# Kernel optimization log

Measured on AMD Instinct MI355X. Metric: run time of the kernel, lower is better.

Reference implementation:

```python
import jax, jax.numpy as jnp
import numpy as np

N_NODES = 100000
N_EDGES = 1600000
DIM_IN, DIM_HID, DIM_OUT = 64, 128, 40


def setup_inputs() -> dict:
    key = jax.random.key(0)
    ks = jax.random.split(key, 6)
    x = jax.random.normal(ks[0], (N_NODES, DIM_IN), dtype=jnp.float32)
    edge_index = jax.random.randint(ks[1], (2, N_EDGES), 0, N_NODES, dtype=jnp.int64)
    s_in = 1.0 / np.sqrt(DIM_IN)
    s_hid = 1.0 / np.sqrt(DIM_HID)
    W1l = jax.random.normal(ks[2], (DIM_HID, DIM_IN), dtype=jnp.float32) * s_in
    W1r = jax.random.normal(ks[3], (DIM_HID, DIM_IN), dtype=jnp.float32) * s_in
    b1 = jnp.zeros((DIM_HID,), dtype=jnp.float32)
    W2l = jax.random.normal(ks[4], (DIM_OUT, DIM_HID), dtype=jnp.float32) * s_hid
    W2r = jax.random.normal(ks[5], (DIM_OUT, DIM_HID), dtype=jnp.float32) * s_hid
    b2 = jnp.zeros((DIM_OUT,), dtype=jnp.float32)
    return {"x": x, "edge_index": edge_index, "W1l": W1l, "b1": b1,
            "W1r": W1r, "W2l": W2l, "b2": b2, "W2r": W2r}


def _sage_conv(h, src, dst, Wl, bl, Wr, n_nodes):
    # mean aggregation of source-node features into target nodes
    msg = h[src]                                      # [E, d]
    agg = jax.ops.segment_sum(msg, dst, num_segments=n_nodes)
    cnt = jax.ops.segment_sum(jnp.ones((src.shape[0],), h.dtype), dst,
                              num_segments=n_nodes)
    agg = agg / jnp.maximum(cnt, 1.0)[:, None]        # [N, d]
    # PyG SAGEConv: lin_l(agg) + bias + lin_r(x) (root weight, no bias)
    return agg @ Wl.T + bl + h @ Wr.T


def reference(x, edge_index, W1l, b1, W1r, W2l, b2, W2r):
    src, dst = edge_index[0], edge_index[1]
    n = x.shape[0]
    h = _sage_conv(x, src, dst, W1l, b1, W1r, n)
    h = jax.nn.relu(h)
    out = _sage_conv(h, src, dst, W2l, b2, W2r, n)
    return jax.nn.log_softmax(out, axis=-1)
```

## Files before the change

kernel.cpp:

```cpp
#include <hip/hip_runtime.h>
#include <math.h>

#define NN 100000
#define DI 64
#define DH 128
#define DO 40

#define NBUCK 512
#define NPB 196
#define CAP 3712
#define CAPP 4352
#define EPB 8192

typedef __attribute__((ext_vector_type(8))) short bf16x8;
typedef __attribute__((ext_vector_type(4))) float f32x4;
typedef __attribute__((ext_vector_type(2))) float f32x2;

__device__ __forceinline__ unsigned short bf16r(float a) {
    unsigned u = __float_as_uint(a);
    u = (u + 0x7FFF + ((u >> 16) & 1)) >> 16;
    return (unsigned short)u;
}
__device__ __forceinline__ unsigned bf16pair(float a, float b) {
    return (unsigned)bf16r(a) | ((unsigned)bf16r(b) << 16);
}
__device__ __forceinline__ float bflo(unsigned u) { return __uint_as_float(u << 16); }
__device__ __forceinline__ float bfhi(unsigned u) { return __uint_as_float(u & 0xFFFF0000u); }

__global__ __launch_bounds__(256) void setup_kernel(
        const float* __restrict__ x, const float* __restrict__ W1l,
        const float* __restrict__ W1r, const float* __restrict__ W2l,
        const float* __restrict__ W2r,
        unsigned* __restrict__ xb, unsigned short* __restrict__ WB1,
        unsigned short* __restrict__ WB2, int* __restrict__ bcur,
        unsigned* __restrict__ p2, int N) {
    int idx = blockIdx.x * 256 + threadIdx.x;
    if (idx < (N + 1) * 32) {
        if (idx < N * 32) {
            float2 f = ((const float2*)x)[idx];
            xb[idx] = bf16pair(f.x, f.y);
        } else {
            xb[idx] = 0;
        }
    }
    if (idx < 16384) {
        int j = idx & 7, lane = (idx >> 3) & 63, ks = (idx >> 9) & 3, nt = idx >> 11;
        int k = ks * 32 + (lane >> 4) * 8 + j;
        int n = nt * 16 + (lane & 15);
        float v = (k < DI) ? W1l[n * DI + k] : W1r[n * DI + (k - DI)];
        WB1[idx] = bf16r(v);
    }
    if (idx >= 16384 && idx < 16384 + 10240) {
        int idx2 = idx - 16384;
        int j = idx2 & 7, lane = (idx2 >> 3) & 63, ks = (idx2 >> 9) & 3, nt = idx2 >> 11;
        int k = ks * 32 + (lane >> 4) * 8 + j;
        int n = nt * 16 + (lane & 15);
        float v = (n < DO) ? W2l[n * DH + k] : W2r[(n - DO) * DH + k];
        WB2[idx2] = bf16r(v);
    }
    if (idx < NBUCK) bcur[idx] = idx * CAP;
    if (idx < 10) p2[(size_t)N * 10 + idx] = 0;
}

__global__ __launch_bounds__(256) void bucket_scatter_kernel(const int* __restrict__ src,
                                                             const int* __restrict__ dst,
                                                             int* __restrict__ bcur,
                                                             int* __restrict__ eb, int E) {
    __shared__ int h[NBUCK];
    int t = threadIdx.x;
    for (int i = t; i < NBUCK; i += 256) h[i] = 0;
    __syncthreads();
    int base = blockIdx.x * EPB;
    int end = base + EPB; if (end > E) end = E;
    for (int i = base + t; i < end; i += 256)
        atomicAdd(&h[(unsigned)dst[i] / NPB], 1);
    __syncthreads();
    for (int i = t; i < NBUCK; i += 256) {
        int v = h[i];
        h[i] = v ? atomicAdd(&bcur[i], v) : 0;
    }
    __syncthreads();
    for (int i = base + t; i < end; i += 256) {
        int d = dst[i];
        unsigned bk = (unsigned)d / NPB;
        int local = d - (int)bk * NPB;
        int pos = atomicAdd(&h[bk], 1);
        eb[pos] = (local << 17) | src[i];
    }
}

__global__ __launch_bounds__(256) void bucket_fill_kernel(const int* __restrict__ eb,
                                                          const int* __restrict__ bend,
                                                          int* __restrict__ rowptr,
                                                          int* __restrict__ cntg,
                                                          float* __restrict__ inv,
                                                          int* __restrict__ col, int N) {
    __shared__ int scnt[256];
    __shared__ int scur[256];
    __shared__ int sbase[256];
    int b = blockIdx.x, t = threadIdx.x;
    int ebeg = b * CAP, eend = bend[b];
    scnt[t] = 0;
    __syncthreads();
    for (int i = ebeg + t; i < eend; i += 256)
        atomicAdd(&scnt[eb[i] >> 17], 1);
    __syncthreads();
    int myc = scnt[t];
    int pc = (myc + 3) & ~3;
    scnt[t] = pc;
    __syncthreads();
    for (int off = 1; off < 256; off <<= 1) {
        int tmp = (t >= off) ? scnt[t - off] : 0;
        __syncthreads();
        scnt[t] += tmp;
        __syncthreads();
    }
    int excl = scnt[t] - pc;
    int base = b * CAPP + excl;
    int node = b * NPB + t;
    if (t < NPB && node < N) {
        rowptr[node] = base;
        cntg[node] = myc;
        inv[node] = 1.0f / (float)(myc > 0 ? myc : 1);
    }
    scur[t] = base;
    sbase[t] = base;
    __syncthreads();
    for (int i = ebeg + t; i < eend; i += 256) {
        int pk = eb[i];
        int pos = atomicAdd(&scur[pk >> 17], 1);
        col[pos] = pk & 0x1FFFF;
    }
    __syncthreads();
    if (t < NPB) {
        int bs = sbase[t];
        for (int i = myc; i < pc; i++) col[bs + i] = NN;
    }
}

__global__ void agg1_kernel(const unsigned* __restrict__ xb, const int* __restrict__ rowptr,
                            const int* __restrict__ cnt, const float* __restrict__ inv,
                            const int* __restrict__ col, unsigned* __restrict__ xa, int N) {
    int n = (blockIdx.x * 256 + threadIdx.x) >> 3;
    int chunk = threadIdx.x & 7;
    if (n >= N) return;
    int beg = rowptr[n], deg = cnt[n];
    int degp = (deg + 3) & ~3;
    float a[8];
#pragma unroll
    for (int j = 0; j < 8; j++) a[j] = 0.f;
    for (int i = 0; i < degp; i += 4) {
        int s0 = col[beg + i], s1 = col[beg + i + 1];
        int s2 = col[beg + i + 2], s3 = col[beg + i + 3];
        uint4 u0 = *(const uint4*)(xb + (size_t)s0 * 32 + chunk * 4);
        uint4 u1 = *(const uint4*)(xb + (size_t)s1 * 32 + chunk * 4);
        uint4 u2 = *(const uint4*)(xb + (size_t)s2 * 32 + chunk * 4);
        uint4 u3 = *(const uint4*)(xb + (size_t)s3 * 32 + chunk * 4);
        a[0] += bflo(u0.x) + bflo(u1.x) + bflo(u2.x) + bflo(u3.x);
        a[1] += bfhi(u0.x) + bfhi(u1.x) + bfhi(u2.x) + bfhi(u3.x);
        a[2] += bflo(u0.y) + bflo(u1.y) + bflo(u2.y) + bflo(u3.y);
        a[3] += bfhi(u0.y) + bfhi(u1.y) + bfhi(u2.y) + bfhi(u3.y);
        a[4] += bflo(u0.z) + bflo(u1.z) + bflo(u2.z) + bflo(u3.z);
        a[5] += bfhi(u0.z) + bfhi(u1.z) + bfhi(u2.z) + bfhi(u3.z);
        a[6] += bflo(u0.w) + bflo(u1.w) + bflo(u2.w) + bflo(u3.w);
        a[7] += bfhi(u0.w) + bfhi(u1.w) + bfhi(u2.w) + bfhi(u3.w);
    }
    float invn = inv[n];
    uint4 o;
    o.x = bf16pair(a[0] * invn, a[1] * invn);
    o.y = bf16pair(a[2] * invn, a[3] * invn);
    o.z = bf16pair(a[4] * invn, a[5] * invn);
    o.w = bf16pair(a[6] * invn, a[7] * invn);
    *(uint4*)(xa + (size_t)n * 64 + chunk * 4) = o;
    uint4 u = *(const uint4*)(xb + (size_t)n * 32 + chunk * 4);
    *(uint4*)(xa + (size_t)n * 64 + 32 + chunk * 4) = u;
}

__global__ __launch_bounds__(256) void gemm1_kernel(const unsigned short* __restrict__ xa,
                                                    const unsigned short* __restrict__ WB1,
                                                    const float* __restrict__ b1,
                                                    unsigned short* __restrict__ h, int N) {
    int w = threadIdx.x >> 6, lane = threadIdx.x & 63;
    int quad = lane >> 4, m = lane & 15;
    int rbase = blockIdx.x * 64 + w * 16;
    int arow = rbase + m; if (arow >= N) arow = N - 1;

    f32x4 acc[8];
#pragma unroll
    for (int nt = 0; nt < 8; nt++) acc[nt] = (f32x4)(0.f);
#pragma unroll
    for (int ks = 0; ks < 4; ks++) {
        bf16x8 a = *(const bf16x8*)(xa + (size_t)arow * 128 + ks * 32 + quad * 8);
#pragma unroll
        for (int nt = 0; nt < 8; nt++) {
            bf16x8 b = *(const bf16x8*)(WB1 + ((size_t)(nt * 4 + ks) * 64 + lane) * 8);
            acc[nt] = __builtin_amdgcn_mfma_f32_16x16x32_bf16(a, b, acc[nt], 0, 0, 0);
        }
    }
#pragma unroll
    for (int nt = 0; nt < 8; nt++) {
        int colj = nt * 16 + m;
        float bj = b1[colj];
#pragma unroll
        for (int r = 0; r < 4; r++) {
            int row = rbase + quad * 4 + r;
            if (row < N) {
                float v = acc[nt][r] + bj;
                h[(size_t)row * 128 + colj] = bf16r(fmaxf(v, 0.f));
            }
        }
    }
}

__global__ __launch_bounds__(256) void gemm2_kernel(const unsigned short* __restrict__ h,
                                                    const unsigned short* __restrict__ WB2,
                                                    const float* __restrict__ b2,
                                                    unsigned* __restrict__ p2,
                                                    float* __restrict__ selfp, int N) {
    __shared__ float st[64][41];
    int w = threadIdx.x >> 6, lane = threadIdx.x & 63;
    int quad = lane >> 4, m = lane & 15;
    int rbase = blockIdx.x * 64 + w * 16;
    int arow = rbase + m; if (arow >= N) arow = N - 1;

    f32x4 acc[5];
#pragma unroll
    for (int nt = 0; nt < 5; nt++) acc[nt] = (f32x4)(0.f);
#pragma unroll
    for (int ks = 0; ks < 4; ks++) {
        bf16x8 a = *(const bf16x8*)(h + (size_t)arow * 128 + ks * 32 + quad * 8);
#pragma unroll
        for (int nt = 0; nt < 5; nt++) {
            bf16x8 b = *(const bf16x8*)(WB2 + ((size_t)(nt * 4 + ks) * 64 + lane) * 8);
            acc[nt] = __builtin_amdgcn_mfma_f32_16x16x32_bf16(a, b, acc[nt], 0, 0, 0);
        }
    }
#pragma unroll
    for (int nt = 0; nt < 5; nt++) {
        int colj = nt * 16 + m;
#pragma unroll
        for (int r = 0; r < 4; r++) {
            int lrow = w * 16 + quad * 4 + r;
            int row = rbase + quad * 4 + r;
            float v = acc[nt][r];
            if (colj < 40) {
                st[lrow][colj] = v;
            } else if (row < N) {
                selfp[(size_t)row * 40 + (colj - 40)] = v + b2[colj - 40];
            }
        }
    }
    __syncthreads();
    for (int i = threadIdx.x; i < 64 * 10; i += 256) {
        int lr = i / 10, dw = i - lr * 10;
        int grow = blockIdx.x * 64 + lr;
        if (grow < N) {
            float v0 = st[lr][dw * 4 + 0], v1 = st[lr][dw * 4 + 1];
            float v2 = st[lr][dw * 4 + 2], v3 = st[lr][dw * 4 + 3];
            unsigned u = __builtin_amdgcn_cvt_pk_fp8_f32(v0, v1, 0u, false);
            u = __builtin_amdgcn_cvt_pk_fp8_f32(v2, v3, u, true);
            p2[(size_t)grow * 10 + dw] = u;
        }
    }
}

__global__ void agg2_softmax_kernel(const unsigned* __restrict__ p2,
                                    const float* __restrict__ selfp,
                                    const int* __restrict__ rowptr,
                                    const int* __restrict__ cnt,
                                    const float* __restrict__ inv,
                                    const int* __restrict__ col,
                                    float* __restrict__ out, int N) {
    int n = (blockIdx.x * 256 + threadIdx.x) >> 3;
    int chunk = threadIdx.x & 7;
    if (n >= N) return;
    int beg = rowptr[n], deg = cnt[n];
    int degp = (deg + 3) & ~3;
    bool vc = (chunk < 5);
    float a[8];
#pragma unroll
    for (int j = 0; j < 8; j++) a[j] = 0.f;
    for (int i = 0; i < degp; i += 4) {
        int s0 = col[beg + i], s1 = col[beg + i + 1];
        int s2 = col[beg + i + 2], s3 = col[beg + i + 3];
        if (vc) {
            uint2 u0 = *(const uint2*)(p2 + (size_t)s0 * 10 + chunk * 2);
            uint2 u1 = *(const uint2*)(p2 + (size_t)s1 * 10 + chunk * 2);
            uint2 u2 = *(const uint2*)(p2 + (size_t)s2 * 10 + chunk * 2);
            uint2 u3 = *(const uint2*)(p2 + (size_t)s3 * 10 + chunk * 2);
            f32x2 d;
            d = __builtin_amdgcn_cvt_pk_f32_fp8(u0.x, false); a[0] += d.x; a[1] += d.y;
            d = __builtin_amdgcn_cvt_pk_f32_fp8(u0.x, true);  a[2] += d.x; a[3] += d.y;
            d = __builtin_amdgcn_cvt_pk_f32_fp8(u0.y, false); a[4] += d.x; a[5] += d.y;
            d = __builtin_amdgcn_cvt_pk_f32_fp8(u0.y, true);  a[6] += d.x; a[7] += d.y;
            d = __builtin_amdgcn_cvt_pk_f32_fp8(u1.x, false); a[0] += d.x; a[1] += d.y;
            d = __builtin_amdgcn_cvt_pk_f32_fp8(u1.x, true);  a[2] += d.x; a[3] += d.y;
            d = __builtin_amdgcn_cvt_pk_f32_fp8(u1.y, false); a[4] += d.x; a[5] += d.y;
            d = __builtin_amdgcn_cvt_pk_f32_fp8(u1.y, true);  a[6] += d.x; a[7] += d.y;
            d = __builtin_amdgcn_cvt_pk_f32_fp8(u2.x, false); a[0] += d.x; a[1] += d.y;
            d = __builtin_amdgcn_cvt_pk_f32_fp8(u2.x, true);  a[2] += d.x; a[3] += d.y;
            d = __builtin_amdgcn_cvt_pk_f32_fp8(u2.y, false); a[4] += d.x; a[5] += d.y;
            d = __builtin_amdgcn_cvt_pk_f32_fp8(u2.y, true);  a[6] += d.x; a[7] += d.y;
            d = __builtin_amdgcn_cvt_pk_f32_fp8(u3.x, false); a[0] += d.x; a[1] += d.y;
            d = __builtin_amdgcn_cvt_pk_f32_fp8(u3.x, true);  a[2] += d.x; a[3] += d.y;
            d = __builtin_amdgcn_cvt_pk_f32_fp8(u3.y, false); a[4] += d.x; a[5] += d.y;
            d = __builtin_amdgcn_cvt_pk_f32_fp8(u3.y, true);  a[6] += d.x; a[7] += d.y;
        }
    }
    float invn = inv[n];
    float v[8];
    if (vc) {
        float4 s0 = *(const float4*)(selfp + (size_t)n * DO + chunk * 8);
        float4 s1 = *(const float4*)(selfp + (size_t)n * DO + chunk * 8 + 4);
        v[0] = a[0] * invn + s0.x; v[1] = a[1] * invn + s0.y;
        v[2] = a[2] * invn + s0.z; v[3] = a[3] * invn + s0.w;
        v[4] = a[4] * invn + s1.x; v[5] = a[5] * invn + s1.y;
        v[6] = a[6] * invn + s1.z; v[7] = a[7] * invn + s1.w;
    } else {
#pragma unroll
        for (int j = 0; j < 8; j++) v[j] = 0.f;
    }
    float mv = -INFINITY;
    if (vc) {
#pragma unroll
        for (int j = 0; j < 8; j++) mv = fmaxf(mv, v[j]);
    }
#pragma unroll
    for (int off = 1; off <= 4; off <<= 1) mv = fmaxf(mv, __shfl_xor(mv, off, 8));
    float es = 0.f;
    if (vc) {
#pragma unroll
        for (int j = 0; j < 8; j++) es += expf(v[j] - mv);
    }
#pragma unroll
    for (int off = 1; off <= 4; off <<= 1) es += __shfl_xor(es, off, 8);
    if (vc) {
        float ls = mv + logf(es);
        float4 o0, o1;
        o0.x = v[0] - ls; o0.y = v[1] - ls; o0.z = v[2] - ls; o0.w = v[3] - ls;
        o1.x = v[4] - ls; o1.y = v[5] - ls; o1.z = v[6] - ls; o1.w = v[7] - ls;
        *(float4*)(out + (size_t)n * DO + chunk * 8) = o0;
        *(float4*)(out + (size_t)n * DO + chunk * 8 + 4) = o1;
    }
}

extern "C" void kernel_launch(void* const* d_in, const int* in_sizes, int n_in,
                              void* d_out, int out_size, void* d_ws, size_t ws_size,
                              hipStream_t stream) {
    const float* x   = (const float*)d_in[0];
    const int*  ei   = (const int*)d_in[1];
    const float* W1l = (const float*)d_in[2];
    const float* b1  = (const float*)d_in[3];
    const float* W1r = (const float*)d_in[4];
    const float* W2l = (const float*)d_in[5];
    const float* b2  = (const float*)d_in[6];
    const float* W2r = (const float*)d_in[7];
    float* out = (float*)d_out;

    const int E = in_sizes[1] / 2;
    const int N = NN;
    const int* src = ei;
    const int* dst = ei + E;
    const int nbe = (E + EPB - 1) / EPB;

    size_t off = 0;
    auto alloc = [&](size_t nf) { size_t o = off; off += (nf + 63) & ~(size_t)63; return o; };
    size_t o_bcur   = alloc(NBUCK);
    size_t o_eb     = alloc((size_t)NBUCK * CAP);
    size_t o_col    = alloc((size_t)NBUCK * CAPP);
    size_t o_rowptr = alloc(N);
    size_t o_cnt    = alloc(N);
    size_t o_inv    = alloc(N);
    size_t o_xb     = alloc((size_t)(N + 1) * 32);
    size_t o_xa     = alloc((size_t)N * 64);
    size_t o_h      = alloc((size_t)N * 64);
    size_t o_p2     = alloc((size_t)(N + 1) * 10);
    size_t o_selfp  = alloc((size_t)N * DO);
    size_t o_wb1    = alloc(16384 / 2);
    size_t o_wb2    = alloc(10240 / 2);
    (void)ws_size;

    float* ws = (float*)d_ws;
    int* bcur   = (int*)(ws + o_bcur);
    int* eb     = (int*)(ws + o_eb);
    int* col    = (int*)(ws + o_col);
    int* rowptr = (int*)(ws + o_rowptr);
    int* cnt    = (int*)(ws + o_cnt);
    float* inv  = ws + o_inv;
    unsigned* xb = (unsigned*)(ws + o_xb);
    unsigned* xa = (unsigned*)(ws + o_xa);
    unsigned short* h   = (unsigned short*)(ws + o_h);
    unsigned* p2 = (unsigned*)(ws + o_p2);
    float* selfp = ws + o_selfp;
    unsigned short* WB1 = (unsigned short*)(ws + o_wb1);
    unsigned short* WB2 = (unsigned short*)(ws + o_wb2);

    setup_kernel<<<((N + 1) * 32 + 255) / 256, 256, 0, stream>>>(
        x, W1l, W1r, W2l, W2r, xb, WB1, WB2, bcur, p2, N);

    bucket_scatter_kernel<<<nbe, 256, 0, stream>>>(src, dst, bcur, eb, E);
    bucket_fill_kernel<<<NBUCK, 256, 0, stream>>>(eb, bcur, rowptr, cnt, inv, col, N);

    agg1_kernel<<<(N * 8 + 255) / 256, 256, 0, stream>>>(xb, rowptr, cnt, inv, col, xa, N);
    gemm1_kernel<<<(N + 63) / 64, 256, 0, stream>>>((const unsigned short*)xa, WB1, b1, h, N);
    gemm2_kernel<<<(N + 63) / 64, 256, 0, stream>>>(h, WB2, b2, p2, selfp, N);
    agg2_softmax_kernel<<<(N * 8 + 255) / 256, 256, 0, stream>>>(p2, selfp, rowptr, cnt, inv, col, out, N);
}
```

Baseline: 230.4 us.

## Fuse setup into bucket scatter and fuse both GEMMs through shared memory

The setup (bf16 conversion, weight packing) and the edge bucket scatter now run as one launch: the first blocks scatter edges, using 512 threads and 4096 edges per block with destinations held in registers, and the remaining blocks do the conversions. bcur becomes a relative counter zeroed by a memset, and the fill kernel adds the bucket base itself. The two GEMMs are fused so the hidden activation h stays in shared memory and is never written to or read back from global memory. This removes two kernel launches and the global round trip of h, at the cost of more shared memory per block in the fused GEMM.

```diff
diff --git a/kernel.cpp b/kernel.cpp
--- a/kernel.cpp
+++ b/kernel.cpp
@@ -10,7 +10,9 @@
 #define NPB 196
 #define CAP 3712
 #define CAPP 4352
-#define EPB 8192
+#define EPB 4096
+#define TPB_S 512
+#define KE (EPB / TPB_S)
 
 typedef __attribute__((ext_vector_type(8))) short bf16x8;
 typedef __attribute__((ext_vector_type(4))) float f32x4;
@@ -27,65 +29,73 @@
 __device__ __forceinline__ float bflo(unsigned u) { return __uint_as_float(u << 16); }
 __device__ __forceinline__ float bfhi(unsigned u) { return __uint_as_float(u & 0xFFFF0000u); }
 
-__global__ __launch_bounds__(256) void setup_kernel(
+__global__ __launch_bounds__(TPB_S) void setup_scatter_kernel(
         const float* __restrict__ x, const float* __restrict__ W1l,
         const float* __restrict__ W1r, const float* __restrict__ W2l,
         const float* __restrict__ W2r,
         unsigned* __restrict__ xb, unsigned short* __restrict__ WB1,
-        unsigned short* __restrict__ WB2, int* __restrict__ bcur,
-        unsigned* __restrict__ p2, int N) {
-    int idx = blockIdx.x * 256 + threadIdx.x;
-    if (idx < (N + 1) * 32) {
-        if (idx < N * 32) {
-            float2 f = ((const float2*)x)[idx];
-            xb[idx] = bf16pair(f.x, f.y);
-        } else {
-            xb[idx] = 0;
-        }
-    }
-    if (idx < 16384) {
-        int j = idx & 7, lane = (idx >> 3) & 63, ks = (idx >> 9) & 3, nt = idx >> 11;
-        int k = ks * 32 + (lane >> 4) * 8 + j;
-        int n = nt * 16 + (lane & 15);
-        float v = (k < DI) ? W1l[n * DI + k] : W1r[n * DI + (k - DI)];
-        WB1[idx] = bf16r(v);
-    }
-    if (idx >= 16384 && idx < 16384 + 10240) {
-        int idx2 = idx - 16384;
-        int j = idx2 & 7, lane = (idx2 >> 3) & 63, ks = (idx2 >> 9) & 3, nt = idx2 >> 11;
-        int k = ks * 32 + (lane >> 4) * 8 + j;
-        int n = nt * 16 + (lane & 15);
-        float v = (n < DO) ? W2l[n * DH + k] : W2r[(n - DO) * DH + k];
-        WB2[idx2] = bf16r(v);
-    }
-    if (idx < NBUCK) bcur[idx] = idx * CAP;
-    if (idx < 10) p2[(size_t)N * 10 + idx] = 0;
-}
-
-__global__ __launch_bounds__(256) void bucket_scatter_kernel(const int* __restrict__ src,
-                                                             const int* __restrict__ dst,
-                                                             int* __restrict__ bcur,
-                                                             int* __restrict__ eb, int E) {
+        unsigned short* __restrict__ WB2, unsigned* __restrict__ p2,
+        const int* __restrict__ src, const int* __restrict__ dst,
+        int* __restrict__ bcur, int* __restrict__ eb,
+        int nbe, int E, int N) {
     __shared__ int h[NBUCK];
     int t = threadIdx.x;
-    for (int i = t; i < NBUCK; i += 256) h[i] = 0;
-    __syncthreads();
-    int base = blockIdx.x * EPB;
-    int end = base + EPB; if (end > E) end = E;
-    for (int i = base + t; i < end; i += 256)
-        atomicAdd(&h[(unsigned)dst[i] / NPB], 1);
-    __syncthreads();
-    for (int i = t; i < NBUCK; i += 256) {
-        int v = h[i];
-        h[i] = v ? atomicAdd(&bcur[i], v) : 0;
-    }
-    __syncthreads();
-    for (int i = base + t; i < end; i += 256) {
-        int d = dst[i];
-        unsigned bk = (unsigned)d / NPB;
-        int local = d - (int)bk * NPB;
-        int pos = atomicAdd(&h[bk], 1);
-        eb[pos] = (local << 17) | src[i];
+    if ((int)blockIdx.x < nbe) {
+        if (t < NBUCK) h[t] = 0;
+        __syncthreads();
+        int base = blockIdx.x * EPB;
+        int end = base + EPB; if (end > E) end = E;
+        int dloc[KE];
+#pragma unroll
+        for (int k = 0; k < KE; k++) {
+            int i = base + t + k * TPB_S;
+            dloc[k] = (i < end) ? dst[i] : -1;
+        }
+#pragma unroll
+        for (int k = 0; k < KE; k++)
+            if (dloc[k] >= 0) atomicAdd(&h[(unsigned)dloc[k] / NPB], 1);
+        __syncthreads();
+        if (t < NBUCK) {
+            int v = h[t];
+            h[t] = v ? (atomicAdd(&bcur[t], v) + t * CAP) : 0;
+        }
+        __syncthreads();
+#pragma unroll
+        for (int k = 0; k < KE; k++) {
+            int d = dloc[k];
+            if (d >= 0) {
+                unsigned bk = (unsigned)d / NPB;
+                int local = d - (int)bk * NPB;
+                int pos = atomicAdd(&h[bk], 1);
+                eb[pos] = (local << 17) | src[base + t + k * TPB_S];
+            }
+        }
+    } else {
+        int idx = (blockIdx.x - nbe) * TPB_S + t;
+        if (idx < (N + 1) * 32) {
+            if (idx < N * 32) {
+                float2 f = ((const float2*)x)[idx];
+                xb[idx] = bf16pair(f.x, f.y);
+            } else {
+                xb[idx] = 0;
+            }
+        }
+        if (idx < 16384) {
+            int j = idx & 7, lane = (idx >> 3) & 63, ks = (idx >> 9) & 3, nt = idx >> 11;
+            int k = ks * 32 + (lane >> 4) * 8 + j;
+            int n = nt * 16 + (lane & 15);
+            float v = (k < DI) ? W1l[n * DI + k] : W1r[n * DI + (k - DI)];
+            WB1[idx] = bf16r(v);
+        }
+        if (idx >= 16384 && idx < 16384 + 10240) {
+            int idx2 = idx - 16384;
+            int j = idx2 & 7, lane = (idx2 >> 3) & 63, ks = (idx2 >> 9) & 3, nt = idx2 >> 11;
+            int k = ks * 32 + (lane >> 4) * 8 + j;
+            int n = nt * 16 + (lane & 15);
+            float v = (n < DO) ? W2l[n * DH + k] : W2r[(n - DO) * DH + k];
+            WB2[idx2] = bf16r(v);
+        }
+        if (idx < 10) p2[(size_t)N * 10 + idx] = 0;
     }
 }
 
@@ -99,7 +109,7 @@
     __shared__ int scur[256];
     __shared__ int sbase[256];
     int b = blockIdx.x, t = threadIdx.x;
-    int ebeg = b * CAP, eend = bend[b];
+    int ebeg = b * CAP, eend = ebeg + bend[b];
     scnt[t] = 0;
     __syncthreads();
     for (int i = ebeg + t; i < eend; i += 256)
@@ -176,63 +186,54 @@
     *(uint4*)(xa + (size_t)n * 64 + 32 + chunk * 4) = u;
 }
 
-__global__ __launch_bounds__(256) void gemm1_kernel(const unsigned short* __restrict__ xa,
-                                                    const unsigned short* __restrict__ WB1,
-                                                    const float* __restrict__ b1,
-                                                    unsigned short* __restrict__ h, int N) {
-    int w = threadIdx.x >> 6, lane = threadIdx.x & 63;
-    int quad = lane >> 4, m = lane & 15;
-    int rbase = blockIdx.x * 64 + w * 16;
-    int arow = rbase + m; if (arow >= N) arow = N - 1;
-
-    f32x4 acc[8];
-#pragma unroll
-    for (int nt = 0; nt < 8; nt++) acc[nt] = (f32x4)(0.f);
-#pragma unroll
-    for (int ks = 0; ks < 4; ks++) {
-        bf16x8 a = *(const bf16x8*)(xa + (size_t)arow * 128 + ks * 32 + quad * 8);
-#pragma unroll
-        for (int nt = 0; nt < 8; nt++) {
-            bf16x8 b = *(const bf16x8*)(WB1 + ((size_t)(nt * 4 + ks) * 64 + lane) * 8);
-            acc[nt] = __builtin_amdgcn_mfma_f32_16x16x32_bf16(a, b, acc[nt], 0, 0, 0);
-        }
-    }
-#pragma unroll
-    for (int nt = 0; nt < 8; nt++) {
-        int colj = nt * 16 + m;
-        float bj = b1[colj];
-#pragma unroll
-        for (int r = 0; r < 4; r++) {
-            int row = rbase + quad * 4 + r;
-            if (row < N) {
-                float v = acc[nt][r] + bj;
-                h[(size_t)row * 128 + colj] = bf16r(fmaxf(v, 0.f));
-            }
-        }
-    }
-}
-
-__global__ __launch_bounds__(256) void gemm2_kernel(const unsigned short* __restrict__ h,
-                                                    const unsigned short* __restrict__ WB2,
-                                                    const float* __restrict__ b2,
-                                                    unsigned* __restrict__ p2,
-                                                    float* __restrict__ selfp, int N) {
+__global__ __launch_bounds__(256) void gemm12_kernel(const unsigned short* __restrict__ xa,
+                                                     const unsigned short* __restrict__ WB1,
+                                                     const float* __restrict__ b1,
+                                                     const unsigned short* __restrict__ WB2,
+                                                     const float* __restrict__ b2,
+                                                     unsigned* __restrict__ p2,
+                                                     float* __restrict__ selfp, int N) {
+    __shared__ unsigned short hs[64][136];
     __shared__ float st[64][41];
     int w = threadIdx.x >> 6, lane = threadIdx.x & 63;
     int quad = lane >> 4, m = lane & 15;
     int rbase = blockIdx.x * 64 + w * 16;
     int arow = rbase + m; if (arow >= N) arow = N - 1;
-
-    f32x4 acc[5];
-#pragma unroll
-    for (int nt = 0; nt < 5; nt++) acc[nt] = (f32x4)(0.f);
+    int lw = w * 16;
+
+    f32x4 acc[8];
+#pragma unroll
+    for (int nt = 0; nt < 8; nt++) acc[nt] = (f32x4)(0.f);
 #pragma unroll
     for (int ks = 0; ks < 4; ks++) {
-        bf16x8 a = *(const bf16x8*)(h + (size_t)arow * 128 + ks * 32 + quad * 8);
+        bf16x8 a = *(const bf16x8*)(xa + (size_t)arow * 128 + ks * 32 + quad * 8);
+#pragma unroll
+        for (int nt = 0; nt < 8; nt++) {
+            bf16x8 b = *(const bf16x8*)(WB1 + ((size_t)(nt * 4 + ks) * 64 + lane) * 8);
+            acc[nt] = __builtin_amdgcn_mfma_f32_16x16x32_bf16(a, b, acc[nt], 0, 0, 0);
+        }
+    }
+#pragma unroll
+    for (int nt = 0; nt < 8; nt++) {
+        int colj = nt * 16 + m;
+        float bj = b1[colj];
+#pragma unroll
+        for (int r = 0; r < 4; r++) {
+            hs[lw + quad * 4 + r][colj] = bf16r(fmaxf(acc[nt][r] + bj, 0.f));
+        }
+    }
+    __syncthreads();
+
+    f32x4 acc2[5];
+#pragma unroll
+    for (int nt = 0; nt < 5; nt++) acc2[nt] = (f32x4)(0.f);
+#pragma unroll
+    for (int ks = 0; ks < 4; ks++) {
+        bf16x8 a = *(const bf16x8*)(&hs[lw + m][ks * 32 + quad * 8]);
 #pragma unroll
         for (int nt = 0; nt < 5; nt++) {
             bf16x8 b = *(const bf16x8*)(WB2 + ((size_t)(nt * 4 + ks) * 64 + lane) * 8);
-            acc[nt] = __builtin_amdgcn_mfma_f32_16x16x32_bf16(a, b, acc[nt], 0, 0, 0);
+            acc2[nt] = __builtin_amdgcn_mfma_f32_16x16x32_bf16(a, b, acc2[nt], 0, 0, 0);
         }
     }
 #pragma unroll
@@ -240,9 +241,9 @@
         int colj = nt * 16 + m;
 #pragma unroll
         for (int r = 0; r < 4; r++) {
-            int lrow = w * 16 + quad * 4 + r;
+            int lrow = lw + quad * 4 + r;
             int row = rbase + quad * 4 + r;
-            float v = acc[nt][r];
+            float v = acc2[nt][r];
             if (colj < 40) {
                 st[lrow][colj] = v;
             } else if (row < N) {
@@ -362,6 +363,7 @@
     const int* src = ei;
     const int* dst = ei + E;
     const int nbe = (E + EPB - 1) / EPB;
+    const int nsetup = ((N + 1) * 32 + TPB_S - 1) / TPB_S;
 
     size_t off = 0;
     auto alloc = [&](size_t nf) { size_t o = off; off += (nf + 63) & ~(size_t)63; return o; };
@@ -373,7 +375,6 @@
     size_t o_inv    = alloc(N);
     size_t o_xb     = alloc((size_t)(N + 1) * 32);
     size_t o_xa     = alloc((size_t)N * 64);
-    size_t o_h      = alloc((size_t)N * 64);
     size_t o_p2     = alloc((size_t)(N + 1) * 10);
     size_t o_selfp  = alloc((size_t)N * DO);
     size_t o_wb1    = alloc(16384 / 2);
@@ -389,20 +390,20 @@
     float* inv  = ws + o_inv;
     unsigned* xb = (unsigned*)(ws + o_xb);
     unsigned* xa = (unsigned*)(ws + o_xa);
-    unsigned short* h   = (unsigned short*)(ws + o_h);
     unsigned* p2 = (unsigned*)(ws + o_p2);
     float* selfp = ws + o_selfp;
     unsigned short* WB1 = (unsigned short*)(ws + o_wb1);
     unsigned short* WB2 = (unsigned short*)(ws + o_wb2);
 
-    setup_kernel<<<((N + 1) * 32 + 255) / 256, 256, 0, stream>>>(
-        x, W1l, W1r, W2l, W2r, xb, WB1, WB2, bcur, p2, N);
-
-    bucket_scatter_kernel<<<nbe, 256, 0, stream>>>(src, dst, bcur, eb, E);
+    hipMemsetAsync(bcur, 0, NBUCK * sizeof(int), stream);
+
+    setup_scatter_kernel<<<nbe + nsetup, TPB_S, 0, stream>>>(
+        x, W1l, W1r, W2l, W2r, xb, WB1, WB2, p2, src, dst, bcur, eb, nbe, E, N);
+
     bucket_fill_kernel<<<NBUCK, 256, 0, stream>>>(eb, bcur, rowptr, cnt, inv, col, N);
 
     agg1_kernel<<<(N * 8 + 255) / 256, 256, 0, stream>>>(xb, rowptr, cnt, inv, col, xa, N);
-    gemm1_kernel<<<(N + 63) / 64, 256, 0, stream>>>((const unsigned short*)xa, WB1, b1, h, N);
-    gemm2_kernel<<<(N + 63) / 64, 256, 0, stream>>>(h, WB2, b2, p2, selfp, N);
+    gemm12_kernel<<<(N + 63) / 64, 256, 0, stream>>>((const unsigned short*)xa, WB1, b1,
+                                                     WB2, b2, p2, selfp, N);
     agg2_softmax_kernel<<<(N * 8 + 255) / 256, 256, 0, stream>>>(p2, selfp, rowptr, cnt, inv, col, out, N);
 }
```

Result: faster. 203.4 us (-11.7%).
